# Kernel optimization log

Measured on AMD Instinct MI355X. Metric: run time of the kernel, lower is better.

## Reference

```python
import jax, jax.numpy as jnp
import numpy as np

N_NODES = 50000
N_EDGES = 800000
D_IN = 64
D_HID = 128  # out_channels * expansion(2)
EPS_MSG = 1e-7
EPS_SOFTMAX = 1e-16
EPS_BN = 1e-5
N_LAYERS = 4


def mish(x):
    return x * jnp.tanh(jax.nn.softplus(x))


def setup_inputs() -> dict:
    key = jax.random.key(0)
    ks = jax.random.split(key, 8)
    x = jax.random.normal(ks[0], (N_NODES, D_IN), dtype=jnp.float32)
    edge_index = jax.random.randint(ks[1], (2, N_EDGES), 0, N_NODES, dtype=jnp.int64)
    # Per-layer GENConv MLP params: Linear(64->128), BN(128), ReLU, Linear(128->64)
    s1 = 1.0 / np.sqrt(D_IN)
    s2 = 1.0 / np.sqrt(D_HID)
    W1 = jax.random.uniform(ks[2], (N_LAYERS, D_IN, D_HID), jnp.float32, -s1, s1)
    b1 = jax.random.uniform(ks[3], (N_LAYERS, D_HID), jnp.float32, -s1, s1)
    gamma = jnp.ones((N_LAYERS, D_HID), jnp.float32)
    beta = jnp.zeros((N_LAYERS, D_HID), jnp.float32)
    W2 = jax.random.uniform(ks[4], (N_LAYERS, D_HID, D_IN), jnp.float32, -s2, s2)
    b2 = jax.random.uniform(ks[5], (N_LAYERS, D_IN), jnp.float32, -s2, s2)
    return {"x": x, "edge_index": edge_index, "W1": W1, "b1": b1,
            "gamma": gamma, "beta": beta, "W2": W2, "b2": b2}


def gen_conv(x, src, dst, W1, b1, gamma, beta, W2, b2):
    n = x.shape[0]
    # message: relu(x_j) + eps  -> [E, D]
    msg = jax.nn.relu(x[src]) + EPS_MSG
    # softmax aggregation (t=1) per destination node, per feature channel
    m = jax.ops.segment_max(msg, dst, num_segments=n)
    e = jnp.exp(msg - m[dst])
    denom = jax.ops.segment_sum(e, dst, num_segments=n)[dst] + EPS_SOFTMAX
    alpha = e / denom
    agg = jax.ops.segment_sum(msg * alpha, dst, num_segments=n)
    # residual with destination features, then 2-layer MLP w/ BatchNorm (train mode)
    h = agg + x
    h = h @ W1 + b1
    mu = jnp.mean(h, axis=0)
    var = jnp.var(h, axis=0)  # biased, as torch BN uses for normalization
    h = (h - mu) * jax.lax.rsqrt(var + EPS_BN) * gamma + beta
    h = jax.nn.relu(h)
    return h @ W2 + b2


def reference(x, edge_index, W1, b1, gamma, beta, W2, b2):
    src, dst = edge_index[0], edge_index[1]
    h = x
    for i in range(N_LAYERS):
        h = gen_conv(h, src, dst, W1[i], b1[i], gamma[i], beta[i], W2[i], b2[i])
        if i < N_LAYERS - 1:
            h = mish(h)
    return h
```

## Files before the change

### kernel.cpp

```cpp
#include <hip/hip_runtime.h>
#include <math.h>

#define N_NODES 50000
#define N_EDGES 800000
#define D_IN 64
#define D_HID 128
#define SCAN_B 256
#define N_SB ((N_NODES + SCAN_B - 1) / SCAN_B)
#define NPB 256
#define NB ((N_NODES + NPB - 1) / NPB)
#define P1_BLOCKS 256
#define EPB (N_EDGES / P1_BLOCKS)

typedef unsigned short u16;
typedef unsigned int u32;
typedef __attribute__((ext_vector_type(8))) short short8;
typedef __attribute__((ext_vector_type(4))) float f32x4;

union U4S8 { uint4 u; short8 s; };

__device__ __forceinline__ float bf2f(u16 u) {
    u32 x = ((u32)u) << 16;
    float f; __builtin_memcpy(&f, &x, 4); return f;
}
__device__ __forceinline__ u16 f2bf(float f) {
    u32 x; __builtin_memcpy(&x, &f, 4);
    x += 0x7fffu + ((x >> 16) & 1u);
    return (u16)(x >> 16);
}
__device__ __forceinline__ u32 pk2(float a, float b) {
    return (u32)f2bf(a) | ((u32)f2bf(b) << 16);
}
__device__ __forceinline__ u32 relu2(u32 w) {
    u32 b = (w >> 15) & 0x00010001u;
    u32 m01 = b ^ 0x00010001u;
    u32 M = (m01 << 16) - m01;
    return w & M;
}


__global__ void count_kernel(const int* __restrict__ dst, int* __restrict__ deg, int E) {
    int i = blockIdx.x * blockDim.x + threadIdx.x;
    if (i < E) atomicAdd(&deg[dst[i]], 1);
}

__global__ __launch_bounds__(SCAN_B) void scan_reduce_kernel(const int* __restrict__ deg,
                                                             int* __restrict__ bsum) {
    __shared__ int s[SCAN_B];
    int i = blockIdx.x * SCAN_B + threadIdx.x;
    int v = (i < N_NODES) ? deg[i] : 0;
    s[threadIdx.x] = v;
    __syncthreads();
    #pragma unroll
    for (int o = SCAN_B / 2; o > 0; o >>= 1) {
        if (threadIdx.x < o) s[threadIdx.x] += s[threadIdx.x + o];
        __syncthreads();
    }
    if (threadIdx.x == 0) bsum[blockIdx.x] = s[0];
}

__global__ __launch_bounds__(SCAN_B) void scan_sums_kernel(const int* __restrict__ bsum,
                                                           int* __restrict__ boff) {
    __shared__ int s[SCAN_B];
    int t = threadIdx.x;
    int v = (t < N_SB) ? bsum[t] : 0;
    s[t] = v;
    __syncthreads();
    #pragma unroll
    for (int o = 1; o < SCAN_B; o <<= 1) {
        int u = (t >= o) ? s[t - o] : 0;
        __syncthreads();
        s[t] += u;
        __syncthreads();
    }
    if (t < N_SB) boff[t] = s[t] - v;
}

__global__ __launch_bounds__(SCAN_B) void scan_write_kernel(const int* __restrict__ deg,
                                                            const int* __restrict__ boff,
                                                            int* __restrict__ off) {
    __shared__ int s[SCAN_B];
    int t = threadIdx.x;
    int i = blockIdx.x * SCAN_B + t;
    int v = (i < N_NODES) ? deg[i] : 0;
    s[t] = v;
    __syncthreads();
    #pragma unroll
    for (int o = 1; o < SCAN_B; o <<= 1) {
        int u = (t >= o) ? s[t - o] : 0;
        __syncthreads();
        s[t] += u;
        __syncthreads();
    }
    int incl = s[t] + boff[blockIdx.x];
    if (i < N_NODES) off[i] = incl - v;
    if (i == N_NODES - 1) off[N_NODES] = incl;
}

__global__ void bin_init_kernel(const int* __restrict__ off, int* __restrict__ gcur,
                                int* __restrict__ esrc) {
    int b = threadIdx.x;
    if (b < NB) gcur[b] = off[min(b * NPB, N_NODES)];
    if (b < 16) esrc[N_EDGES + b] = 0;
}

__global__ __launch_bounds__(256) void bin_pass1_kernel(const int* __restrict__ src,
                                                        const int* __restrict__ dst,
                                                        int* __restrict__ gcur,
                                                        int2* __restrict__ ebuf) {
    __shared__ int hist[NB];
    __shared__ int base[NB];
    const int tid = threadIdx.x;
    const int e0 = blockIdx.x * EPB, e1 = e0 + EPB;
    for (int b = tid; b < NB; b += 256) hist[b] = 0;
    __syncthreads();
    for (int i = e0 + tid; i < e1; i += 256)
        atomicAdd(&hist[dst[i] >> 8], 1);
    __syncthreads();
    for (int b = tid; b < NB; b += 256) {
        base[b] = atomicAdd(&gcur[b], hist[b]);
        hist[b] = 0;
    }
    __syncthreads();
    for (int i = e0 + tid; i < e1; i += 256) {
        int d = dst[i];
        int b = d >> 8;
        int slot = base[b] + atomicAdd(&hist[b], 1);
        ebuf[slot] = make_int2(src[i], d);
    }
}

__global__ __launch_bounds__(256) void bin_pass2_kernel(const int* __restrict__ off,
                                                        const int2* __restrict__ ebuf,
                                                        int* __restrict__ esrc) {
    __shared__ int soff[NPB];
    __shared__ int cur[NPB];
    const int b = blockIdx.x;
    const int tid = threadIdx.x;
    const int n0 = b * NPB;
    soff[tid] = off[min(n0 + tid, N_NODES)];
    cur[tid] = 0;
    __syncthreads();
    const int e0 = soff[0];
    const int e1 = off[min(n0 + NPB, N_NODES)];
    for (int i = e0 + tid; i < e1; i += 256) {
        int2 p = ebuf[i];
        int dl = p.y - n0;
        int slot = soff[dl] + atomicAdd(&cur[dl], 1);
        esrc[slot] = p.x;
    }
}

__global__ __launch_bounds__(256) void xcvt_kernel(const float* __restrict__ x,
                                                   u16* __restrict__ xb,
                                                   u16* __restrict__ rb) {
    int i = blockIdx.x * 256 + threadIdx.x;
    if (i < N_NODES * D_IN / 4) {
        float4 v = ((const float4*)x)[i];
        u32 lo = pk2(v.x, v.y), hi = pk2(v.z, v.w);
        ((uint2*)xb)[i] = make_uint2(lo, hi);
        ((uint2*)rb)[i] = make_uint2(relu2(lo), relu2(hi));
    }
}

__global__ __launch_bounds__(256) void wprep_kernel(const float* __restrict__ W1,
                                                    const float* __restrict__ W2,
                                                    u16* __restrict__ w1f,
                                                    u16* __restrict__ w2f) {
    const int b = blockIdx.x;
    const int L = b >> 1;
    if ((b & 1) == 0) {
        const float* W = W1 + (size_t)L * 64 * 128;
        u16* outp = w1f + (size_t)L * 8192;
        for (int idx = threadIdx.x; idx < 1024; idx += 256) {
            int ln = idx & 63, th = idx >> 6;
            int half = th & 1, t = th >> 1;
            int k0 = half * 32 + (ln >> 4) * 8;
            int n = t * 16 + (ln & 15);
            uint4 o;
            o.x = pk2(W[(k0 + 0) * 128 + n], W[(k0 + 1) * 128 + n]);
            o.y = pk2(W[(k0 + 2) * 128 + n], W[(k0 + 3) * 128 + n]);
            o.z = pk2(W[(k0 + 4) * 128 + n], W[(k0 + 5) * 128 + n]);
            o.w = pk2(W[(k0 + 6) * 128 + n], W[(k0 + 7) * 128 + n]);
            *(uint4*)&outp[(size_t)idx * 8] = o;
        }
    } else {
        const float* W = W2 + (size_t)L * 128 * 64;
        u16* outp = w2f + (size_t)L * 8192;
        for (int idx = threadIdx.x; idx < 1024; idx += 256) {
            int ln = idx & 63, th = idx >> 6;
            int ks = th & 3, t = th >> 2;
            int k0 = ks * 32 + (ln >> 4) * 8;
            int n = t * 16 + (ln & 15);
            uint4 o;
            o.x = pk2(W[(k0 + 0) * 64 + n], W[(k0 + 1) * 64 + n]);
            o.y = pk2(W[(k0 + 2) * 64 + n], W[(k0 + 3) * 64 + n]);
            o.z = pk2(W[(k0 + 4) * 64 + n], W[(k0 + 5) * 64 + n]);
            o.w = pk2(W[(k0 + 6) * 64 + n], W[(k0 + 7) * 64 + n]);
            *(uint4*)&outp[(size_t)idx * 8] = o;
        }
    }
}

__global__ __launch_bounds__(256) void agg_kernel(const u16* __restrict__ xb,
                                                  const u16* __restrict__ rb,
                                                  const int* __restrict__ off,
                                                  const int* __restrict__ esrc,
                                                  u16* __restrict__ h) {
    const int node = blockIdx.x * 4 + (threadIdx.x >> 6);
    const int ln = threadIdx.x & 63;
    const int jb = __builtin_amdgcn_readfirstlane(off[node]);
    const int je = __builtin_amdgcn_readfirstlane(off[node + 1]);
    const float xown = bf2f(xb[(size_t)node * 64 + ln]);
    float s0 = 0.f, s1 = 0.f, t0 = 0.f, t1 = 0.f;
    int j = jb;
    const int nfull = (je - jb) >> 4;
    for (int it = 0; it < nfull; ++it, j += 16) {
        #pragma unroll
        for (int kk = 0; kk < 16; kk += 2) {
            int i0 = esrc[j + kk];
            int i1 = esrc[j + kk + 1];
            float m0 = bf2f(rb[(size_t)i0 * 64 + ln]);
            float m1 = bf2f(rb[(size_t)i1 * 64 + ln]);
            float p0 = __expf(m0);
            float p1 = __expf(m1);
            s0 += p0; t0 = fmaf(m0, p0, t0);
            s1 += p1; t1 = fmaf(m1, p1, t1);
        }
    }
    const int rem = je - j;
    if (rem > 0) {
        #pragma unroll
        for (int kk = 0; kk < 16; kk += 2) {
            int i0 = esrc[j + kk];
            int i1 = esrc[j + kk + 1];
            float m0 = bf2f(rb[(size_t)i0 * 64 + ln]);
            float m1 = bf2f(rb[(size_t)i1 * 64 + ln]);
            float p0 = (kk < rem)     ? __expf(m0) : 0.f;
            float p1 = (kk + 1 < rem) ? __expf(m1) : 0.f;
            s0 += p0; t0 = fmaf(m0, p0, t0);
            s1 += p1; t1 = fmaf(m1, p1, t1);
        }
    }
    const float s = s0 + s1, t = t0 + t1;
    const float v = t / (s + 1e-16f) + 1e-7f + xown;
    h[(size_t)node * 64 + ln] = f2bf(v);
}

#define SC1 136
__global__ __launch_bounds__(256) void gemm1_kernel(const u16* __restrict__ A,
                                                    const u16* __restrict__ Wf,
                                                    const float* __restrict__ bias,
                                                    u16* __restrict__ Bout,
                                                    float* __restrict__ S,
                                                    float* __restrict__ Q) {
    __shared__ u16 sC[64 * SC1];
    __shared__ float sRed[2][4][128];
    const int tid = threadIdx.x;
    const int wave = tid >> 6, ln = tid & 63;
    const int lm = ln & 15, quad = ln >> 4;
    const int row0g = blockIdx.x * 64;
    const int row0 = row0g + wave * 16;
    const int rA = min(row0 + lm, N_NODES - 1);

    U4S8 a0, a1;
    a0.u = *(const uint4*)&A[(size_t)rA * 64 + quad * 8];
    a1.u = *(const uint4*)&A[(size_t)rA * 64 + 32 + quad * 8];

    f32x4 acc[8];
    #pragma unroll
    for (int t = 0; t < 8; t++) {
        float b = bias[t * 16 + lm];
        acc[t] = (f32x4){b, b, b, b};
    }
    #pragma unroll
    for (int t = 0; t < 8; t++) {
        U4S8 b0, b1;
        b0.u = *(const uint4*)&Wf[(size_t)((t * 2 + 0) * 64 + ln) * 8];
        b1.u = *(const uint4*)&Wf[(size_t)((t * 2 + 1) * 64 + ln) * 8];
        acc[t] = __builtin_amdgcn_mfma_f32_16x16x32_bf16(a0.s, b0.s, acc[t], 0, 0, 0);
        acc[t] = __builtin_amdgcn_mfma_f32_16x16x32_bf16(a1.s, b1.s, acc[t], 0, 0, 0);
    }
    const int rbase = row0 + quad * 4;
    #pragma unroll
    for (int t = 0; t < 8; t++) {
        float ss = 0.f, qq = 0.f;
        #pragma unroll
        for (int rg = 0; rg < 4; rg++) {
            if (rbase + rg < N_NODES) {
                float v = acc[t][rg];
                ss += v; qq = fmaf(v, v, qq);
            }
        }
        ss += __shfl_xor(ss, 16); ss += __shfl_xor(ss, 32);
        qq += __shfl_xor(qq, 16); qq += __shfl_xor(qq, 32);
        if (quad == 0) {
            sRed[0][wave][t * 16 + lm] = ss;
            sRed[1][wave][t * 16 + lm] = qq;
        }
    }
    const int lr0 = wave * 16 + quad * 4;
    #pragma unroll
    for (int t = 0; t < 8; t++) {
        #pragma unroll
        for (int rg = 0; rg < 4; rg++)
            sC[(lr0 + rg) * SC1 + t * 16 + lm] = f2bf(acc[t][rg]);
    }
    __syncthreads();
    const int c8 = (tid & 15) * 8;
    #pragma unroll
    for (int i = 0; i < 4; i++) {
        int lr = (tid >> 4) + i * 16;
        int r = row0g + lr;
        if (r < N_NODES)
            *(uint4*)&Bout[(size_t)r * 128 + c8] = *(const uint4*)&sC[lr * SC1 + c8];
    }
    if (tid < 128) {
        float v = sRed[0][0][tid] + sRed[0][1][tid] + sRed[0][2][tid] + sRed[0][3][tid];
        atomicAdd(&S[tid], v);
    } else {
        int c = tid - 128;
        float v = sRed[1][0][c] + sRed[1][1][c] + sRed[1][2][c] + sRed[1][3][c];
        atomicAdd(&Q[c], v);
    }
}

__device__ __forceinline__ float mish_f(float v) {
    if (v > 30.f) return v;
    float u = __expf(v);
    float t = (u + 1.f) * (u + 1.f);
    return v * (t - 1.f) / (t + 1.f);
}

#define SC2B 72
#define SC2F 68
__global__ __launch_bounds__(256) void gemm2_kernel(const u16* __restrict__ H,
                                                    const float* __restrict__ S,
                                                    const float* __restrict__ Q,
                                                    const float* __restrict__ gamma,
                                                    const float* __restrict__ beta,
                                                    const u16* __restrict__ Wf,
                                                    const float* __restrict__ bias,
                                                    float* __restrict__ outf,
                                                    u16* __restrict__ xb,
                                                    u16* __restrict__ rb,
                                                    int dobf16) {
    __shared__ float sss[256];
    __shared__ __align__(16) char sCraw[64 * SC2F * 4];
    u16* sCb = (u16*)sCraw;
    float* sCf = (float*)sCraw;
    const int tid = threadIdx.x;
    if (tid < 128) {
        float mean = S[tid] * (1.f / N_NODES);
        float var = fmaxf(Q[tid] * (1.f / N_NODES) - mean * mean, 0.f);
        float sc = gamma[tid] * rsqrtf(var + 1e-5f);
        sss[tid] = sc;
        sss[128 + tid] = beta[tid] - mean * sc;
    }
    __syncthreads();
    const int wave = tid >> 6, ln = tid & 63;
    const int lm = ln & 15, quad = ln >> 4;
    const int row0g = blockIdx.x * 64;
    const int row0 = row0g + wave * 16;
    const int rA = min(row0 + lm, N_NODES - 1);

    f32x4 acc[4];
    #pragma unroll
    for (int t = 0; t < 4; t++) {
        float b = bias[t * 16 + lm];
        acc[t] = (f32x4){b, b, b, b};
    }
    #pragma unroll
    for (int ks = 0; ks < 4; ks++) {
        const int k0 = ks * 32 + quad * 8;
        U4S8 h8;
        h8.u = *(const uint4*)&H[(size_t)rA * 128 + k0];
        U4S8 a;
        #pragma unroll
        for (int j2 = 0; j2 < 4; j2++) {
            int k = k0 + 2 * j2;
            float v0 = fmaxf(fmaf(bf2f((u16)h8.s[2 * j2]),     sss[k],     sss[128 + k]),     0.f);
            float v1 = fmaxf(fmaf(bf2f((u16)h8.s[2 * j2 + 1]), sss[k + 1], sss[128 + k + 1]), 0.f);
            ((u32*)&a.u)[j2] = pk2(v0, v1);
        }
        #pragma unroll
        for (int t = 0; t < 4; t++) {
            U4S8 b;
            b.u = *(const uint4*)&Wf[(size_t)((t * 4 + ks) * 64 + ln) * 8];
            acc[t] = __builtin_amdgcn_mfma_f32_16x16x32_bf16(a.s, b.s, acc[t], 0, 0, 0);
        }
    }
    const int lr0 = wave * 16 + quad * 4;
    if (dobf16) {
        #pragma unroll
        for (int t = 0; t < 4; t++) {
            #pragma unroll
            for (int rg = 0; rg < 4; rg++)
                sCb[(lr0 + rg) * SC2B + t * 16 + lm] = f2bf(mish_f(acc[t][rg]));
        }
        __syncthreads();
        const int c8 = (tid & 7) * 8;
        #pragma unroll
        for (int i = 0; i < 2; i++) {
            int lr = (tid >> 3) + i * 32;
            int r = row0g + lr;
            if (r < N_NODES) {
                uint4 val = *(const uint4*)&sCb[lr * SC2B + c8];
                *(uint4*)&xb[(size_t)r * 64 + c8] = val;
                uint4 rv;
                rv.x = relu2(val.x); rv.y = relu2(val.y);
                rv.z = relu2(val.z); rv.w = relu2(val.w);
                *(uint4*)&rb[(size_t)r * 64 + c8] = rv;
            }
        }
    } else {
        #pragma unroll
        for (int t = 0; t < 4; t++) {
            #pragma unroll
            for (int rg = 0; rg < 4; rg++)
                sCf[(lr0 + rg) * SC2F + t * 16 + lm] = acc[t][rg];
        }
        __syncthreads();
        const int c8 = (tid & 7) * 8;
        #pragma unroll
        for (int i = 0; i < 2; i++) {
            int lr = (tid >> 3) + i * 32;
            int r = row0g + lr;
            if (r < N_NODES) {
                *(float4*)&outf[(size_t)r * 64 + c8]     = *(const float4*)&sCf[lr * SC2F + c8];
                *(float4*)&outf[(size_t)r * 64 + c8 + 4] = *(const float4*)&sCf[lr * SC2F + c8 + 4];
            }
        }
    }
}


extern "C" void kernel_launch(void* const* d_in, const int* in_sizes, int n_in,
                              void* d_out, int out_size, void* d_ws, size_t ws_size,
                              hipStream_t stream) {
    const float* x     = (const float*)d_in[0];
    const int*   ei    = (const int*)d_in[1];
    const float* W1    = (const float*)d_in[2];
    const float* b1    = (const float*)d_in[3];
    const float* gamma = (const float*)d_in[4];
    const float* beta  = (const float*)d_in[5];
    const float* W2    = (const float*)d_in[6];
    const float* b2    = (const float*)d_in[7];
    float* out = (float*)d_out;

    const int* src = ei;
    const int* dst = ei + N_EDGES;

    char* base = (char*)d_ws;
    size_t o = 0;
    auto take = [&](size_t bytes) -> char* {
        char* p = base + o;
        o = (o + bytes + 255) & ~(size_t)255;
        return p;
    };
    int* deg     = (int*)take((size_t)N_NODES * 4);
    int* off     = (int*)take((size_t)(N_NODES + 1) * 4);
    int* esrc    = (int*)take((size_t)(N_EDGES + 16) * 4);
    int2* ebuf   = (int2*)take((size_t)N_EDGES * 8);
    int* bsum    = (int*)take((size_t)N_SB * 4);
    int* boff    = (int*)take((size_t)N_SB * 4);
    int* gcur    = (int*)take((size_t)NB * 4);
    float* bn    = (float*)take(1024 * 4);
    u16* w1f     = (u16*)take((size_t)4 * 8192 * 2);
    u16* w2f     = (u16*)take((size_t)4 * 8192 * 2);
    u16* xbuf    = (u16*)take((size_t)N_NODES * D_IN * 2);
    u16* rbuf    = (u16*)take((size_t)N_NODES * D_IN * 2);
    u16* hbuf    = (u16*)take((size_t)N_NODES * D_IN * 2);
    u16* h1buf   = (u16*)take((size_t)N_NODES * D_HID * 2);

    hipMemsetAsync(deg, 0, (size_t)N_NODES * 4, stream);
    hipMemsetAsync(bn, 0, 1024 * 4, stream);
    count_kernel<<<(N_EDGES + 255) / 256, 256, 0, stream>>>(dst, deg, N_EDGES);
    scan_reduce_kernel<<<N_SB, SCAN_B, 0, stream>>>(deg, bsum);
    scan_sums_kernel<<<1, SCAN_B, 0, stream>>>(bsum, boff);
    scan_write_kernel<<<N_SB, SCAN_B, 0, stream>>>(deg, boff, off);
    bin_init_kernel<<<1, 256, 0, stream>>>(off, gcur, esrc);
    bin_pass1_kernel<<<P1_BLOCKS, 256, 0, stream>>>(src, dst, gcur, ebuf);
    bin_pass2_kernel<<<NB, 256, 0, stream>>>(off, ebuf, esrc);
    xcvt_kernel<<<(N_NODES * D_IN / 4 + 255) / 256, 256, 0, stream>>>(x, xbuf, rbuf);
    wprep_kernel<<<8, 256, 0, stream>>>(W1, W2, w1f, w2f);

    const int NBLK = (N_NODES + 63) / 64;
    const int ABLK = (N_NODES + 3) / 4;
    for (int L = 0; L < 4; L++) {
        float* Sb = bn + L * 256;
        float* Qb = Sb + 128;
        agg_kernel<<<ABLK, 256, 0, stream>>>(xbuf, rbuf, off, esrc, hbuf);
        gemm1_kernel<<<NBLK, 256, 0, stream>>>(
            hbuf, w1f + (size_t)L * 8192, b1 + (size_t)L * D_HID, h1buf,
            Sb, Qb);
        gemm2_kernel<<<NBLK, 256, 0, stream>>>(
            h1buf, Sb, Qb, gamma + (size_t)L * D_HID, beta + (size_t)L * D_HID,
            w2f + (size_t)L * 8192, b2 + (size_t)L * D_IN,
            out, xbuf, rbuf, (L < 3) ? 1 : 0);
    }
}
```

Measured before the change: 400.6 us.

## Merge preprocessing kernels and pack edge pairs into 32-bit words

Cuts the setup launch count by folding the bn memset and esrc padding into count_kernel and computing gcur inside scan_write. Bin pass 2, the x conversion and the weight prep now run as one kernel partitioned by block index. The binned edge buffer packs src and dst as 16-bit halves of one u32, which halves its traffic. That packing only works because node ids fit in 16 bits, which N_NODES=50000 satisfies. The gcur value equals the block offset since NPB equals SCAN_B.

```diff
diff --git a/kernel.cpp b/kernel.cpp
--- a/kernel.cpp
+++ b/kernel.cpp
@@ -11,6 +11,7 @@
 #define NB ((N_NODES + NPB - 1) / NPB)
 #define P1_BLOCKS 256
 #define EPB (N_EDGES / P1_BLOCKS)
+#define XCVT_B (N_NODES * D_IN / 4 / 256)
 
 typedef unsigned short u16;
 typedef unsigned int u32;
@@ -39,9 +40,15 @@
 }
 
 
-__global__ void count_kernel(const int* __restrict__ dst, int* __restrict__ deg, int E) {
+__global__ void count_kernel(const int* __restrict__ dst, int* __restrict__ deg,
+                             float* __restrict__ bn, int* __restrict__ esrc) {
     int i = blockIdx.x * blockDim.x + threadIdx.x;
-    if (i < E) atomicAdd(&deg[dst[i]], 1);
+    if (i < N_EDGES) atomicAdd(&deg[dst[i]], 1);
+    if (blockIdx.x == 0) {
+        int t = threadIdx.x;
+        ((float4*)bn)[t] = make_float4(0.f, 0.f, 0.f, 0.f);
+        if (t < 16) esrc[N_EDGES + t] = 0;
+    }
 }
 
 __global__ __launch_bounds__(SCAN_B) void scan_reduce_kernel(const int* __restrict__ deg,
@@ -78,7 +85,8 @@
 
 __global__ __launch_bounds__(SCAN_B) void scan_write_kernel(const int* __restrict__ deg,
                                                             const int* __restrict__ boff,
-                                                            int* __restrict__ off) {
+                                                            int* __restrict__ off,
+                                                            int* __restrict__ gcur) {
     __shared__ int s[SCAN_B];
     int t = threadIdx.x;
     int i = blockIdx.x * SCAN_B + t;
@@ -95,19 +103,13 @@
     int incl = s[t] + boff[blockIdx.x];
     if (i < N_NODES) off[i] = incl - v;
     if (i == N_NODES - 1) off[N_NODES] = incl;
-}
-
-__global__ void bin_init_kernel(const int* __restrict__ off, int* __restrict__ gcur,
-                                int* __restrict__ esrc) {
-    int b = threadIdx.x;
-    if (b < NB) gcur[b] = off[min(b * NPB, N_NODES)];
-    if (b < 16) esrc[N_EDGES + b] = 0;
+    if (t == 0) gcur[blockIdx.x] = boff[blockIdx.x];
 }
 
 __global__ __launch_bounds__(256) void bin_pass1_kernel(const int* __restrict__ src,
                                                         const int* __restrict__ dst,
                                                         int* __restrict__ gcur,
-                                                        int2* __restrict__ ebuf) {
+                                                        u32* __restrict__ ebuf) {
     __shared__ int hist[NB];
     __shared__ int base[NB];
     const int tid = threadIdx.x;
@@ -126,53 +128,53 @@
         int d = dst[i];
         int b = d >> 8;
         int slot = base[b] + atomicAdd(&hist[b], 1);
-        ebuf[slot] = make_int2(src[i], d);
-    }
-}
-
-__global__ __launch_bounds__(256) void bin_pass2_kernel(const int* __restrict__ off,
-                                                        const int2* __restrict__ ebuf,
-                                                        int* __restrict__ esrc) {
-    __shared__ int soff[NPB];
-    __shared__ int cur[NPB];
-    const int b = blockIdx.x;
+        ebuf[slot] = ((u32)src[i] << 16) | (u32)d;
+    }
+}
+
+__global__ __launch_bounds__(256) void p2xw_kernel(const int* __restrict__ off,
+                                                   const u32* __restrict__ ebuf,
+                                                   int* __restrict__ esrc,
+                                                   const float* __restrict__ x,
+                                                   u16* __restrict__ xb,
+                                                   u16* __restrict__ rb,
+                                                   const float* __restrict__ W1,
+                                                   const float* __restrict__ W2,
+                                                   u16* __restrict__ w1f,
+                                                   u16* __restrict__ w2f) {
     const int tid = threadIdx.x;
-    const int n0 = b * NPB;
-    soff[tid] = off[min(n0 + tid, N_NODES)];
-    cur[tid] = 0;
-    __syncthreads();
-    const int e0 = soff[0];
-    const int e1 = off[min(n0 + NPB, N_NODES)];
-    for (int i = e0 + tid; i < e1; i += 256) {
-        int2 p = ebuf[i];
-        int dl = p.y - n0;
-        int slot = soff[dl] + atomicAdd(&cur[dl], 1);
-        esrc[slot] = p.x;
-    }
-}
-
-__global__ __launch_bounds__(256) void xcvt_kernel(const float* __restrict__ x,
-                                                   u16* __restrict__ xb,
-                                                   u16* __restrict__ rb) {
-    int i = blockIdx.x * 256 + threadIdx.x;
-    if (i < N_NODES * D_IN / 4) {
+    if (blockIdx.x < NB) {
+        __shared__ int soff[NPB];
+        __shared__ int cur[NPB];
+        const int b = blockIdx.x;
+        const int n0 = b * NPB;
+        soff[tid] = off[min(n0 + tid, N_NODES)];
+        cur[tid] = 0;
+        __syncthreads();
+        const int e0 = soff[0];
+        const int e1 = off[min(n0 + NPB, N_NODES)];
+        for (int i = e0 + tid; i < e1; i += 256) {
+            u32 p = ebuf[i];
+            int dl = (int)(p & 0xFFFFu) - n0;
+            int slot = soff[dl] + atomicAdd(&cur[dl], 1);
+            esrc[slot] = (int)(p >> 16);
+        }
+        return;
+    }
+    if (blockIdx.x < NB + XCVT_B) {
+        int i = (blockIdx.x - NB) * 256 + tid;
         float4 v = ((const float4*)x)[i];
         u32 lo = pk2(v.x, v.y), hi = pk2(v.z, v.w);
         ((uint2*)xb)[i] = make_uint2(lo, hi);
         ((uint2*)rb)[i] = make_uint2(relu2(lo), relu2(hi));
-    }
-}
-
-__global__ __launch_bounds__(256) void wprep_kernel(const float* __restrict__ W1,
-                                                    const float* __restrict__ W2,
-                                                    u16* __restrict__ w1f,
-                                                    u16* __restrict__ w2f) {
-    const int b = blockIdx.x;
+        return;
+    }
+    const int b = blockIdx.x - NB - XCVT_B;
     const int L = b >> 1;
     if ((b & 1) == 0) {
         const float* W = W1 + (size_t)L * 64 * 128;
         u16* outp = w1f + (size_t)L * 8192;
-        for (int idx = threadIdx.x; idx < 1024; idx += 256) {
+        for (int idx = tid; idx < 1024; idx += 256) {
             int ln = idx & 63, th = idx >> 6;
             int half = th & 1, t = th >> 1;
             int k0 = half * 32 + (ln >> 4) * 8;
@@ -187,7 +189,7 @@
     } else {
         const float* W = W2 + (size_t)L * 128 * 64;
         u16* outp = w2f + (size_t)L * 8192;
-        for (int idx = threadIdx.x; idx < 1024; idx += 256) {
+        for (int idx = tid; idx < 1024; idx += 256) {
             int ln = idx & 63, th = idx >> 6;
             int ks = th & 3, t = th >> 2;
             int k0 = ks * 32 + (ln >> 4) * 8;
@@ -461,7 +463,7 @@
     int* deg     = (int*)take((size_t)N_NODES * 4);
     int* off     = (int*)take((size_t)(N_NODES + 1) * 4);
     int* esrc    = (int*)take((size_t)(N_EDGES + 16) * 4);
-    int2* ebuf   = (int2*)take((size_t)N_EDGES * 8);
+    u32* ebuf    = (u32*)take((size_t)N_EDGES * 4);
     int* bsum    = (int*)take((size_t)N_SB * 4);
     int* boff    = (int*)take((size_t)N_SB * 4);
     int* gcur    = (int*)take((size_t)NB * 4);
@@ -474,16 +476,14 @@
     u16* h1buf   = (u16*)take((size_t)N_NODES * D_HID * 2);
 
     hipMemsetAsync(deg, 0, (size_t)N_NODES * 4, stream);
-    hipMemsetAsync(bn, 0, 1024 * 4, stream);
-    count_kernel<<<(N_EDGES + 255) / 256, 256, 0, stream>>>(dst, deg, N_EDGES);
+    count_kernel<<<(N_EDGES + 255) / 256, 256, 0, stream>>>(dst, deg, bn, esrc);
     scan_reduce_kernel<<<N_SB, SCAN_B, 0, stream>>>(deg, bsum);
     scan_sums_kernel<<<1, SCAN_B, 0, stream>>>(bsum, boff);
-    scan_write_kernel<<<N_SB, SCAN_B, 0, stream>>>(deg, boff, off);
-    bin_init_kernel<<<1, 256, 0, stream>>>(off, gcur, esrc);
+    scan_write_kernel<<<N_SB, SCAN_B, 0, stream>>>(deg, boff, off, gcur);
     bin_pass1_kernel<<<P1_BLOCKS, 256, 0, stream>>>(src, dst, gcur, ebuf);
-    bin_pass2_kernel<<<NB, 256, 0, stream>>>(off, ebuf, esrc);
-    xcvt_kernel<<<(N_NODES * D_IN / 4 + 255) / 256, 256, 0, stream>>>(x, xbuf, rbuf);
-    wprep_kernel<<<8, 256, 0, stream>>>(W1, W2, w1f, w2f);
+    p2xw_kernel<<<NB + XCVT_B + 8, 256, 0, stream>>>(off, ebuf, esrc,
+                                                     x, xbuf, rbuf,
+                                                     W1, W2, w1f, w2f);
 
     const int NBLK = (N_NODES + 63) / 64;
     const int ABLK = (N_NODES + 3) / 4;
```

After: 391.7 us. 2.2% less time.
